# Performance work log

Measured on AMD Instinct MI355X. Metric: run time of the kernel, lower is better.

## Reference

```python
import jax, jax.numpy as jnp
import numpy as np

D_MODEL = 1024
NUM_HEADS = 16
D_K = D_MODEL // NUM_HEADS
B, S = 2, 2048


def setup_inputs() -> dict:
    key = jax.random.key(0)
    ks = jax.random.split(key, 11)
    s = 1.0 / np.sqrt(D_MODEL)
    inp = {
        "Q": jax.random.normal(ks[0], (B, S, D_MODEL), jnp.float32),
        "K": jax.random.normal(ks[1], (B, S, D_MODEL), jnp.float32),
        "V": jax.random.normal(ks[2], (B, S, D_MODEL), jnp.float32),
        "Wq": jax.random.uniform(ks[3], (D_MODEL, D_MODEL), jnp.float32, -s, s),
        "bq": jax.random.uniform(ks[4], (D_MODEL,), jnp.float32, -s, s),
        "Wk": jax.random.uniform(ks[5], (D_MODEL, D_MODEL), jnp.float32, -s, s),
        "bk": jax.random.uniform(ks[6], (D_MODEL,), jnp.float32, -s, s),
        "Wv": jax.random.uniform(ks[7], (D_MODEL, D_MODEL), jnp.float32, -s, s),
        "bv": jax.random.uniform(ks[8], (D_MODEL,), jnp.float32, -s, s),
        "Wo": jax.random.uniform(ks[9], (D_MODEL, D_MODEL), jnp.float32, -s, s),
        "bo": jax.random.uniform(ks[10], (D_MODEL,), jnp.float32, -s, s),
    }
    return inp


def _split_heads(x):
    b, s, _ = x.shape
    return x.reshape(b, s, NUM_HEADS, D_K).transpose(0, 2, 1, 3)  # [B,H,S,Dk]


def reference(Q, K, V, Wq, bq, Wk, bk, Wv, bv, Wo, bo):
    q = _split_heads(Q @ Wq.T + bq)
    k = _split_heads(K @ Wk.T + bk)
    v = _split_heads(V @ Wv.T + bv)
    scale = 1.0 / jnp.sqrt(jnp.asarray(D_K, q.dtype))
    scores = jnp.einsum("bhqd,bhkd->bhqk", q, k) * scale  # [B,H,S,S]
    attn = jax.nn.softmax(scores, axis=-1)
    out = jnp.einsum("bhqk,bhkd->bhqd", attn, v)
    out = out.transpose(0, 2, 1, 3).reshape(Q.shape[0], -1, D_MODEL)
    return out @ Wo.T + bo
```

## Files before the change

kernel.cpp:

```cpp
#include <hip/hip_runtime.h>
#include <stdint.h>

typedef __bf16 bf16;
typedef __bf16 bf16x8 __attribute__((ext_vector_type(8)));
typedef float floatx4 __attribute__((ext_vector_type(4)));

#define S_LEN 2048
#define DM 1024
#define NH 16
#define DK 64
#define MTOT 4096

__device__ __forceinline__ void gll16(const void* g, void* l) {
  __builtin_amdgcn_global_load_lds(
      (const __attribute__((address_space(1))) void*)g,
      (__attribute__((address_space(3))) void*)l, 16, 0, 0);
}

__global__ __launch_bounds__(256) void cvt_kernel(
    const float* __restrict__ Wq, const float* __restrict__ Wk, const float* __restrict__ Wv,
    const float* __restrict__ Xq, const float* __restrict__ Xk,
    bf16* __restrict__ wqb, bf16* __restrict__ wkb, bf16* __restrict__ wvb,
    bf16* __restrict__ xqb, bf16* __restrict__ xkb)
{
  const int c = blockIdx.x;
  const float* src; bf16* dst; int off;
  if      (c < 512)  { src = Wq; dst = wqb; off = c; }
  else if (c < 1024) { src = Wk; dst = wkb; off = c - 512; }
  else if (c < 1536) { src = Wv; dst = wvb; off = c - 1024; }
  else if (c < 3584) { src = Xq; dst = xqb; off = c - 1536; }
  else               { src = Xk; dst = xkb; off = c - 3584; }
  const size_t base = (size_t)off * 2048 + threadIdx.x * 8;
  float4 a = *(const float4*)(src + base);
  float4 b = *(const float4*)(src + base + 4);
  bf16x8 h;
  h[0] = (bf16)a.x; h[1] = (bf16)a.y; h[2] = (bf16)a.z; h[3] = (bf16)a.w;
  h[4] = (bf16)b.x; h[5] = (bf16)b.y; h[6] = (bf16)b.z; h[7] = (bf16)b.w;
  *(bf16x8*)(dst + base) = h;
}

__global__ __launch_bounds__(256) void proj_qk_kernel(
    const bf16* __restrict__ xqb, const bf16* __restrict__ xkb,
    const bf16* __restrict__ wqb, const bf16* __restrict__ wkb,
    const float* __restrict__ bqp, const float* __restrict__ bkp,
    bf16* __restrict__ qb, bf16* __restrict__ kb)
{
  const int bid = blockIdx.x;
  const int xcd = bid & 7;
  const int slot = bid >> 3;
  const int m_blk = xcd * 4 + (slot & 3);
  const int n_blk = (slot >> 2) & 7;
  const int z = slot >> 5;

  const bf16* X     = z ? xkb : xqb;
  const bf16* W     = z ? wkb : wqb;
  const float* bias = z ? bkp : bqp;

  const int m0 = m_blk * 128;
  const int n0 = n_blk * 128;
  const int tid = threadIdx.x;
  const int lane = tid & 63;
  const int wid = tid >> 6;
  const int wm = (wid & 1) * 64;
  const int wn = (wid >> 1) * 64;

  __shared__ bf16 As[2][128 * 64];
  __shared__ bf16 Bs[2][128 * 64];

  floatx4 acc[4][4];
  #pragma unroll
  for (int i = 0; i < 4; i++)
    #pragma unroll
    for (int j = 0; j < 4; j++) acc[i][j] = (floatx4){0.f, 0.f, 0.f, 0.f};

  const int mr = lane & 15;
  const int q4 = lane >> 4;
  const int r8_in = lane >> 3, cb8_ph = lane & 7;

  #define STAGE_QK(buf, kt)                                                   \
    {                                                                         \
      _Pragma("unroll")                                                       \
      for (int j = 0; j < 4; j++) {                                           \
        const int c = wid * 4 + j;                                            \
        const int row = c * 8 + r8_in;                                        \
        const int cb = cb8_ph ^ (row & 7);                                    \
        gll16(X + (size_t)(m0 + row) * DM + (kt) + cb * 8, &As[buf][c * 512]);\
      }                                                                       \
      _Pragma("unroll")                                                       \
      for (int j = 0; j < 4; j++) {                                           \
        const int c = wid * 4 + j;                                            \
        const int row = c * 8 + r8_in;                                        \
        const int cb = cb8_ph ^ (row & 7);                                    \
        gll16(W + (size_t)(n0 + row) * DM + (kt) + cb * 8, &Bs[buf][c * 512]);\
      }                                                                       \
    }

  STAGE_QK(0, 0);
  int cur = 0;
  for (int kt = 0; kt < DM; kt += 64) {
    if (kt + 64 < DM) {
      STAGE_QK(cur ^ 1, kt + 64);
      asm volatile("s_waitcnt vmcnt(8)" ::: "memory");
    } else {
      asm volatile("s_waitcnt vmcnt(0)" ::: "memory");
    }
    __builtin_amdgcn_s_barrier();

    #pragma unroll
    for (int kk = 0; kk < 2; kk++) {
      bf16x8 af[4], bfr[4];
      #pragma unroll
      for (int mt = 0; mt < 4; mt++) {
        const int row = wm + mt * 16 + mr;
        const int cb = 4 * kk + q4;
        af[mt] = *(const bf16x8*)&As[cur][row * 64 + (cb ^ (row & 7)) * 8];
      }
      #pragma unroll
      for (int nt = 0; nt < 4; nt++) {
        const int row = wn + nt * 16 + mr;
        const int cb = 4 * kk + q4;
        bfr[nt] = *(const bf16x8*)&Bs[cur][row * 64 + (cb ^ (row & 7)) * 8];
      }
      #pragma unroll
      for (int mt = 0; mt < 4; mt++)
        #pragma unroll
        for (int nt = 0; nt < 4; nt++)
          acc[mt][nt] = __builtin_amdgcn_mfma_f32_16x16x32_bf16(af[mt], bfr[nt], acc[mt][nt], 0, 0, 0);
    }

    __builtin_amdgcn_s_barrier();
    cur ^= 1;
  }
  #undef STAGE_QK

  const float qscale = (z == 0) ? 0.125f : 1.0f;
  bf16* dst = (z == 0) ? qb : kb;
  #pragma unroll
  for (int nt = 0; nt < 4; nt++) {
    const int gn = n0 + wn + nt * 16 + mr;
    const float bv = bias[gn];
    const int h = gn >> 6, d = gn & 63;
    #pragma unroll
    for (int mt = 0; mt < 4; mt++) {
      const int mbase = m0 + wm + mt * 16 + q4 * 4;
      #pragma unroll
      for (int r = 0; r < 4; r++) {
        const int gm = mbase + r;
        const int bi = gm >> 11, s = gm & 2047;
        const bf16 hv = (bf16)((acc[mt][nt][r] + bv) * qscale);
        dst[(((size_t)(bi * NH + h)) * S_LEN + s) * DK + d] = hv;
      }
    }
  }
}

__global__ __launch_bounds__(256) void proj_v_kernel(
    const float* __restrict__ Xv, const bf16* __restrict__ wvb,
    const float* __restrict__ bvp, bf16* __restrict__ vtb)
{
  const int bid = blockIdx.x;
  const int xcd = bid & 7;
  const int slot = bid >> 3;
  const int m_blk = xcd * 4 + (slot & 3);
  const int n_blk = slot >> 2;

  const int m0 = m_blk * 128;
  const int n0 = n_blk * 128;
  const int tid = threadIdx.x;
  const int lane = tid & 63;
  const int wid = tid >> 6;
  const int wm = (wid & 1) * 64;
  const int wn = (wid >> 1) * 64;

  __shared__ float Asf[2][128 * 64];
  __shared__ bf16  Bs[2][128 * 64];

  floatx4 acc[4][4];
  #pragma unroll
  for (int i = 0; i < 4; i++)
    #pragma unroll
    for (int j = 0; j < 4; j++) acc[i][j] = (floatx4){0.f, 0.f, 0.f, 0.f};

  const int mr = lane & 15;
  const int q4 = lane >> 4;
  const int r8_in = lane >> 3, cb8_ph = lane & 7;
  const int r4_in = lane >> 4, cb16_ph = lane & 15;

  #define STAGE_V(buf, kt)                                                     \
    {                                                                          \
      _Pragma("unroll")                                                        \
      for (int j = 0; j < 8; j++) {                                            \
        const int c = wid * 8 + j;                                             \
        const int row = c * 4 + r4_in;                                         \
        const int cb = cb16_ph ^ (row & 7);                                    \
        gll16(Xv + (size_t)(m0 + row) * DM + (kt) + cb * 4, &Asf[buf][c * 256]);\
      }                                                                        \
      _Pragma("unroll")                                                        \
      for (int j = 0; j < 4; j++) {                                            \
        const int c = wid * 4 + j;                                             \
        const int row = c * 8 + r8_in;                                         \
        const int cb = cb8_ph ^ (row & 7);                                     \
        gll16(wvb + (size_t)(n0 + row) * DM + (kt) + cb * 8, &Bs[buf][c * 512]);\
      }                                                                        \
    }

  STAGE_V(0, 0);
  int cur = 0;
  for (int kt = 0; kt < DM; kt += 64) {
    if (kt + 64 < DM) {
      STAGE_V(cur ^ 1, kt + 64);
      asm volatile("s_waitcnt vmcnt(12)" ::: "memory");
    } else {
      asm volatile("s_waitcnt vmcnt(0)" ::: "memory");
    }
    __builtin_amdgcn_s_barrier();

    #pragma unroll
    for (int kk = 0; kk < 2; kk++) {
      bf16x8 af[4], bfr[4];
      #pragma unroll
      for (int mt = 0; mt < 4; mt++) {
        const int row = wm + mt * 16 + mr;
        const int cb0 = 8 * kk + 2 * q4;
        const float4 lo = *(const float4*)&Asf[cur][row * 64 + (cb0 ^ (row & 7)) * 4];
        const float4 hi = *(const float4*)&Asf[cur][row * 64 + ((cb0 + 1) ^ (row & 7)) * 4];
        bf16x8 a;
        a[0] = (bf16)lo.x; a[1] = (bf16)lo.y; a[2] = (bf16)lo.z; a[3] = (bf16)lo.w;
        a[4] = (bf16)hi.x; a[5] = (bf16)hi.y; a[6] = (bf16)hi.z; a[7] = (bf16)hi.w;
        af[mt] = a;
      }
      #pragma unroll
      for (int nt = 0; nt < 4; nt++) {
        const int row = wn + nt * 16 + mr;
        const int cb = 4 * kk + q4;
        bfr[nt] = *(const bf16x8*)&Bs[cur][row * 64 + (cb ^ (row & 7)) * 8];
      }
      #pragma unroll
      for (int mt = 0; mt < 4; mt++)
        #pragma unroll
        for (int nt = 0; nt < 4; nt++)
          acc[mt][nt] = __builtin_amdgcn_mfma_f32_16x16x32_bf16(af[mt], bfr[nt], acc[mt][nt], 0, 0, 0);
    }

    __builtin_amdgcn_s_barrier();
    cur ^= 1;
  }
  #undef STAGE_V

  #pragma unroll
  for (int nt = 0; nt < 4; nt++) {
    const int gn = n0 + wn + nt * 16 + mr;
    const float bv = bvp[gn];
    const int h = gn >> 6, d = gn & 63;
    #pragma unroll
    for (int mt = 0; mt < 4; mt++) {
      const int mbase = m0 + wm + mt * 16 + q4 * 4;
      #pragma unroll
      for (int r = 0; r < 4; r++) {
        const int gm = mbase + r;
        const int bi = gm >> 11, s = gm & 2047;
        vtb[(((size_t)(bi * NH + h)) * DK + d) * S_LEN + s] = (bf16)(acc[mt][nt][r] + bv);
      }
    }
  }
}

__global__ __launch_bounds__(256) void attn_kernel(
    const bf16* __restrict__ qb, const bf16* __restrict__ kb,
    const bf16* __restrict__ vtb, bf16* __restrict__ ob)
{
  const int bid = blockIdx.x;
  const int xcd = bid & 7;
  const int slot = bid >> 3;
  const int bh = xcd * 4 + (slot & 3);
  const int qt = slot >> 2;

  const int tid = threadIdx.x;
  const int lane = tid & 63;
  const int wid = tid >> 6;

  const bf16* qh = qb + (size_t)bh * S_LEN * DK;
  const bf16* kh = kb + (size_t)bh * S_LEN * DK;
  const bf16* vh = vtb + (size_t)bh * DK * S_LEN;

  __shared__ bf16 Ks[128 * 64];
  __shared__ bf16 Vs[64 * 128];
  __shared__ bf16 Ps[4][32][136];

  const int mr = lane & 15;
  const int q4 = lane >> 4;

  bf16x8 aq[2][2];
  #pragma unroll
  for (int mt = 0; mt < 2; mt++)
    #pragma unroll
    for (int kk = 0; kk < 2; kk++)
      aq[mt][kk] = *(const bf16x8*)(qh + (size_t)(qt * 128 + wid * 32 + mt * 16 + mr) * DK + kk * 32 + q4 * 8);

  floatx4 acc_o[2][4];
  #pragma unroll
  for (int mt = 0; mt < 2; mt++)
    #pragma unroll
    for (int dt = 0; dt < 4; dt++) acc_o[mt][dt] = (floatx4){0.f, 0.f, 0.f, 0.f};
  float l_p[2][4] = {{0.f,0.f,0.f,0.f},{0.f,0.f,0.f,0.f}};

  const int r8_in = lane >> 3, cb8_ph = lane & 7;
  const int r4_in = lane >> 4, cb16_ph = lane & 15;

  for (int it = 0; it < S_LEN / 128; it++) {
    const int s0 = it * 128;
    __syncthreads();
    #pragma unroll
    for (int j = 0; j < 4; j++) {
      const int c = wid * 4 + j;
      const int row = c * 8 + r8_in;
      const int cb = cb8_ph ^ (row & 7);
      gll16(kh + (size_t)(s0 + row) * DK + cb * 8, &Ks[c * 512]);
    }
    #pragma unroll
    for (int j = 0; j < 4; j++) {
      const int c = wid * 4 + j;
      const int row = c * 4 + r4_in;
      const int cb = cb16_ph ^ (row & 7);
      gll16(vh + (size_t)row * S_LEN + s0 + cb * 8, &Vs[c * 512]);
    }
    __syncthreads();

    floatx4 sc[2][8];
    #pragma unroll
    for (int mt = 0; mt < 2; mt++)
      #pragma unroll
      for (int i = 0; i < 8; i++) sc[mt][i] = (floatx4){0.f, 0.f, 0.f, 0.f};
    #pragma unroll
    for (int kk = 0; kk < 2; kk++) {
      #pragma unroll
      for (int nt = 0; nt < 8; nt++) {
        const int row = nt * 16 + mr;
        const int cb = kk * 4 + q4;
        bf16x8 b = *(const bf16x8*)&Ks[row * 64 + (cb ^ (row & 7)) * 8];
        #pragma unroll
        for (int mt = 0; mt < 2; mt++)
          sc[mt][nt] = __builtin_amdgcn_mfma_f32_16x16x32_bf16(aq[mt][kk], b, sc[mt][nt], 0, 0, 0);
      }
    }

    #pragma unroll
    for (int mt = 0; mt < 2; mt++)
      #pragma unroll
      for (int nt = 0; nt < 8; nt++)
        #pragma unroll
        for (int r = 0; r < 4; r++) {
          const float pv = __expf(sc[mt][nt][r]);
          l_p[mt][r] += pv;
          Ps[wid][mt * 16 + q4 * 4 + r][nt * 16 + mr] = (bf16)pv;
        }

    #pragma unroll
    for (int kk2 = 0; kk2 < 4; kk2++) {
      bf16x8 ap[2];
      #pragma unroll
      for (int mt = 0; mt < 2; mt++)
        ap[mt] = *(const bf16x8*)&Ps[wid][mt * 16 + mr][kk2 * 32 + q4 * 8];
      #pragma unroll
      for (int dt = 0; dt < 4; dt++) {
        const int row = dt * 16 + mr;
        const int cb = kk2 * 4 + q4;
        bf16x8 b = *(const bf16x8*)&Vs[row * 128 + (cb ^ (row & 7)) * 8];
        #pragma unroll
        for (int mt = 0; mt < 2; mt++)
          acc_o[mt][dt] = __builtin_amdgcn_mfma_f32_16x16x32_bf16(ap[mt], b, acc_o[mt][dt], 0, 0, 0);
      }
    }
  }

  const int bi = bh >> 4, h = bh & 15;
  #pragma unroll
  for (int mt = 0; mt < 2; mt++) {
    float inv[4];
    #pragma unroll
    for (int r = 0; r < 4; r++) {
      float v = l_p[mt][r];
      #pragma unroll
      for (int off = 1; off < 16; off <<= 1) v += __shfl_xor(v, off, 16);
      inv[r] = 1.0f / v;
    }
    #pragma unroll
    for (int dt = 0; dt < 4; dt++) {
      const int d = dt * 16 + mr;
      #pragma unroll
      for (int r = 0; r < 4; r++) {
        const int s = qt * 128 + wid * 32 + mt * 16 + q4 * 4 + r;
        ob[((size_t)(bi * S_LEN + s)) * DM + h * DK + d] = (bf16)(acc_o[mt][dt][r] * inv[r]);
      }
    }
  }
}

__global__ __launch_bounds__(256) void oproj_kernel(
    const bf16* __restrict__ X, const float* __restrict__ W,
    const float* __restrict__ bias, float* __restrict__ out)
{
  const int bid = blockIdx.x;
  const int xcd = bid & 7;
  const int slot = bid >> 3;
  const int m0 = (xcd * 4 + (slot & 3)) * 128;
  const int n0 = (slot >> 2) * 64;

  const int tid = threadIdx.x;
  const int lane = tid & 63;
  const int wid = tid >> 6;
  const int wm = wid * 32;

  __shared__ bf16  As[2][128 * 64];
  __shared__ float Bsf[2][64 * 64];

  floatx4 acc[2][4];
  #pragma unroll
  for (int i = 0; i < 2; i++)
    #pragma unroll
    for (int j = 0; j < 4; j++) acc[i][j] = (floatx4){0.f, 0.f, 0.f, 0.f};

  const int mr = lane & 15;
  const int q4 = lane >> 4;

  const int r8_in = lane >> 3, cb8_ph = lane & 7;
  const int r4_in = lane >> 4, cb16_ph = lane & 15;

  #define STAGE_O(buf, kt)                                                    \
    {                                                                         \
      _Pragma("unroll")                                                       \
      for (int j = 0; j < 4; j++) {                                           \
        const int c = wid * 4 + j;                                            \
        const int row = c * 8 + r8_in;                                        \
        const int cb = cb8_ph ^ (row & 7);                                    \
        gll16(X + (size_t)(m0 + row) * DM + (kt) + cb * 8, &As[buf][c * 512]);\
      }                                                                       \
      _Pragma("unroll")                                                       \
      for (int j = 0; j < 4; j++) {                                           \
        const int c = wid * 4 + j;                                            \
        const int row = c * 4 + r4_in;                                        \
        const int cb = cb16_ph ^ (row & 7);                                   \
        gll16(W + (size_t)(n0 + row) * DM + (kt) + cb * 4, &Bsf[buf][c * 256]);\
      }                                                                       \
    }

  STAGE_O(0, 0);
  int cur = 0;
  for (int kt = 0; kt < DM; kt += 64) {
    if (kt + 64 < DM) {
      STAGE_O(cur ^ 1, kt + 64);
      asm volatile("s_waitcnt vmcnt(8)" ::: "memory");
    } else {
      asm volatile("s_waitcnt vmcnt(0)" ::: "memory");
    }
    __builtin_amdgcn_s_barrier();

    #pragma unroll
    for (int kk = 0; kk < 2; kk++) {
      bf16x8 af[2], bfr[4];
      #pragma unroll
      for (int mt = 0; mt < 2; mt++) {
        const int row = wm + mt * 16 + mr;
        const int cb = 4 * kk + q4;
        af[mt] = *(const bf16x8*)&As[cur][row * 64 + (cb ^ (row & 7)) * 8];
      }
      #pragma unroll
      for (int nt = 0; nt < 4; nt++) {
        const int row = nt * 16 + mr;
        const int cb0 = 8 * kk + 2 * q4;
        const float4 lo = *(const float4*)&Bsf[cur][row * 64 + (cb0 ^ (row & 7)) * 4];
        const float4 hi = *(const float4*)&Bsf[cur][row * 64 + ((cb0 + 1) ^ (row & 7)) * 4];
        bf16x8 b;
        b[0] = (bf16)lo.x; b[1] = (bf16)lo.y; b[2] = (bf16)lo.z; b[3] = (bf16)lo.w;
        b[4] = (bf16)hi.x; b[5] = (bf16)hi.y; b[6] = (bf16)hi.z; b[7] = (bf16)hi.w;
        bfr[nt] = b;
      }
      #pragma unroll
      for (int mt = 0; mt < 2; mt++)
        #pragma unroll
        for (int nt = 0; nt < 4; nt++)
          acc[mt][nt] = __builtin_amdgcn_mfma_f32_16x16x32_bf16(af[mt], bfr[nt], acc[mt][nt], 0, 0, 0);
    }

    __builtin_amdgcn_s_barrier();
    cur ^= 1;
  }
  #undef STAGE_O

  #pragma unroll
  for (int nt = 0; nt < 4; nt++) {
    const int gn = n0 + nt * 16 + mr;
    const float bv = bias[gn];
    #pragma unroll
    for (int mt = 0; mt < 2; mt++) {
      const int mbase = m0 + wm + mt * 16 + q4 * 4;
      #pragma unroll
      for (int r = 0; r < 4; r++)
        out[(size_t)(mbase + r) * DM + gn] = acc[mt][nt][r] + bv;
    }
  }
}

extern "C" void kernel_launch(void* const* d_in, const int* in_sizes, int n_in,
                              void* d_out, int out_size, void* d_ws, size_t ws_size,
                              hipStream_t stream) {
  const float* Q  = (const float*)d_in[0];
  const float* K  = (const float*)d_in[1];
  const float* V  = (const float*)d_in[2];
  const float* Wq = (const float*)d_in[3];
  const float* bq = (const float*)d_in[4];
  const float* Wk = (const float*)d_in[5];
  const float* bk = (const float*)d_in[6];
  const float* Wv = (const float*)d_in[7];
  const float* bv = (const float*)d_in[8];
  const float* Wo = (const float*)d_in[9];
  const float* bo = (const float*)d_in[10];
  float* out = (float*)d_out;

  const size_t NE = (size_t)MTOT * DM;
  bf16* qb  = (bf16*)d_ws;
  bf16* kb  = qb + NE;
  bf16* vtb = kb + NE;
  bf16* ao  = vtb + NE;
  bf16* wqb = ao;
  bf16* wkb = ao + (size_t)DM * DM;
  bf16* wvb = ao + 2 * (size_t)DM * DM;
  bf16* xqb = (bf16*)d_out;
  bf16* xkb = xqb + NE;

  cvt_kernel<<<dim3(5632), 256, 0, stream>>>(Wq, Wk, Wv, Q, K, wqb, wkb, wvb, xqb, xkb);
  proj_qk_kernel<<<dim3(512), 256, 0, stream>>>(xqb, xkb, wqb, wkb, bq, bk, qb, kb);
  proj_v_kernel<<<dim3(256), 256, 0, stream>>>(V, wvb, bv, vtb);
  attn_kernel<<<dim3(512), 256, 0, stream>>>(qb, kb, vtb, ao);
  oproj_kernel<<<dim3(512), 256, 0, stream>>>(ao, Wo, bo, out);
}
```

Baseline: 248.9 us.

## Double-buffer K/V tiles in attention and stream P through a small per-wave buffer

Adds two LDS buffers each for K and V, so the next key/value tile is fetched asynchronously with global_load_lds while the current tile is computed. Explicit vmcnt waits and raw barriers replace the two __syncthreads per iteration. Softmax exponentiation is moved into the PV loop, staging only a 32-column chunk of P per wave instead of the full 128-column tile. This is meant to hide global load latency behind MFMA work and shrink the P buffer. In exchange it roughly doubles K/V LDS usage, which could lower occupancy, and it relies on hand-written wait counts being correct.

```diff
diff --git a/kernel.cpp b/kernel.cpp
--- a/kernel.cpp
+++ b/kernel.cpp
@@ -283,9 +283,9 @@
   const bf16* kh = kb + (size_t)bh * S_LEN * DK;
   const bf16* vh = vtb + (size_t)bh * DK * S_LEN;
 
-  __shared__ bf16 Ks[128 * 64];
-  __shared__ bf16 Vs[64 * 128];
-  __shared__ bf16 Ps[4][32][136];
+  __shared__ bf16 Ks[2][128 * 64];
+  __shared__ bf16 Vs[2][64 * 128];
+  __shared__ bf16 Psc[4][32][40];
 
   const int mr = lane & 15;
   const int q4 = lane >> 4;
@@ -307,24 +307,34 @@
   const int r8_in = lane >> 3, cb8_ph = lane & 7;
   const int r4_in = lane >> 4, cb16_ph = lane & 15;
 
+  #define STAGE_A(buf, s0)                                                    \
+    {                                                                         \
+      _Pragma("unroll")                                                       \
+      for (int j = 0; j < 4; j++) {                                           \
+        const int c = wid * 4 + j;                                            \
+        const int row = c * 8 + r8_in;                                        \
+        const int cb = cb8_ph ^ (row & 7);                                    \
+        gll16(kh + (size_t)((s0) + row) * DK + cb * 8, &Ks[buf][c * 512]);    \
+      }                                                                       \
+      _Pragma("unroll")                                                       \
+      for (int j = 0; j < 4; j++) {                                           \
+        const int c = wid * 4 + j;                                            \
+        const int row = c * 4 + r4_in;                                        \
+        const int cb = cb16_ph ^ (row & 7);                                   \
+        gll16(vh + (size_t)row * S_LEN + (s0) + cb * 8, &Vs[buf][c * 512]);   \
+      }                                                                       \
+    }
+
+  STAGE_A(0, 0);
+  int cur = 0;
   for (int it = 0; it < S_LEN / 128; it++) {
-    const int s0 = it * 128;
-    __syncthreads();
-    #pragma unroll
-    for (int j = 0; j < 4; j++) {
-      const int c = wid * 4 + j;
-      const int row = c * 8 + r8_in;
-      const int cb = cb8_ph ^ (row & 7);
-      gll16(kh + (size_t)(s0 + row) * DK + cb * 8, &Ks[c * 512]);
-    }
-    #pragma unroll
-    for (int j = 0; j < 4; j++) {
-      const int c = wid * 4 + j;
-      const int row = c * 4 + r4_in;
-      const int cb = cb16_ph ^ (row & 7);
-      gll16(vh + (size_t)row * S_LEN + s0 + cb * 8, &Vs[c * 512]);
-    }
-    __syncthreads();
+    if (it + 1 < S_LEN / 128) {
+      STAGE_A(cur ^ 1, (it + 1) * 128);
+      asm volatile("s_waitcnt vmcnt(8)" ::: "memory");
+    } else {
+      asm volatile("s_waitcnt vmcnt(0)" ::: "memory");
+    }
+    __builtin_amdgcn_s_barrier();
 
     floatx4 sc[2][8];
     #pragma unroll
@@ -337,7 +347,7 @@
       for (int nt = 0; nt < 8; nt++) {
         const int row = nt * 16 + mr;
         const int cb = kk * 4 + q4;
-        bf16x8 b = *(const bf16x8*)&Ks[row * 64 + (cb ^ (row & 7)) * 8];
+        bf16x8 b = *(const bf16x8*)&Ks[cur][row * 64 + (cb ^ (row & 7)) * 8];
         #pragma unroll
         for (int mt = 0; mt < 2; mt++)
           sc[mt][nt] = __builtin_amdgcn_mfma_f32_16x16x32_bf16(aq[mt][kk], b, sc[mt][nt], 0, 0, 0);
@@ -345,33 +355,36 @@
     }
 
     #pragma unroll
-    for (int mt = 0; mt < 2; mt++)
-      #pragma unroll
-      for (int nt = 0; nt < 8; nt++)
+    for (int kk2 = 0; kk2 < 4; kk2++) {
+      #pragma unroll
+      for (int mt = 0; mt < 2; mt++)
         #pragma unroll
-        for (int r = 0; r < 4; r++) {
-          const float pv = __expf(sc[mt][nt][r]);
-          l_p[mt][r] += pv;
-          Ps[wid][mt * 16 + q4 * 4 + r][nt * 16 + mr] = (bf16)pv;
-        }
-
-    #pragma unroll
-    for (int kk2 = 0; kk2 < 4; kk2++) {
+        for (int nt2 = 0; nt2 < 2; nt2++)
+          #pragma unroll
+          for (int r = 0; r < 4; r++) {
+            const float pv = __expf(sc[mt][kk2 * 2 + nt2][r]);
+            l_p[mt][r] += pv;
+            Psc[wid][mt * 16 + q4 * 4 + r][nt2 * 16 + mr] = (bf16)pv;
+          }
       bf16x8 ap[2];
       #pragma unroll
       for (int mt = 0; mt < 2; mt++)
-        ap[mt] = *(const bf16x8*)&Ps[wid][mt * 16 + mr][kk2 * 32 + q4 * 8];
+        ap[mt] = *(const bf16x8*)&Psc[wid][mt * 16 + mr][q4 * 8];
       #pragma unroll
       for (int dt = 0; dt < 4; dt++) {
         const int row = dt * 16 + mr;
         const int cb = kk2 * 4 + q4;
-        bf16x8 b = *(const bf16x8*)&Vs[row * 128 + (cb ^ (row & 7)) * 8];
+        bf16x8 b = *(const bf16x8*)&Vs[cur][row * 128 + (cb ^ (row & 7)) * 8];
         #pragma unroll
         for (int mt = 0; mt < 2; mt++)
           acc_o[mt][dt] = __builtin_amdgcn_mfma_f32_16x16x32_bf16(ap[mt], b, acc_o[mt][dt], 0, 0, 0);
       }
     }
-  }
+
+    __builtin_amdgcn_s_barrier();
+    cur ^= 1;
+  }
+  #undef STAGE_A
 
   const int bi = bh >> 4, h = bh & 15;
   #pragma unroll
```

Result: no change. 248.7 us (-0.1%).
